# Kernel tuning notes

Hardware: AMD Instinct MI355X
Metric: run time of the kernel (lower is better)

The kernel has to match this reference:

```python
import jax, jax.numpy as jnp
import numpy as np

B, S, D_IN, D_QK, D_V = 4, 4096, 1024, 64, 64

def setup_inputs() -> dict:
    key = jax.random.key(0)
    ks = jax.random.split(key, 8)
    sd = 1.0 / np.sqrt(D_IN)
    return {
        "X": jax.random.normal(ks[0], (B, S, D_IN), dtype=jnp.float32),
        "mask": jnp.ones((B, S, 1), dtype=jnp.float32),
        "Wq": jax.random.uniform(ks[1], (D_IN, D_QK), jnp.float32, -sd, sd),
        "bq": jax.random.uniform(ks[2], (D_QK,), jnp.float32, -sd, sd),
        "Wk": jax.random.uniform(ks[3], (D_IN, D_QK), jnp.float32, -sd, sd),
        "bk": jax.random.uniform(ks[4], (D_QK,), jnp.float32, -sd, sd),
        "Wv": jax.random.uniform(ks[5], (D_IN, D_V), jnp.float32, -sd, sd),
        "bv": jax.random.uniform(ks[6], (D_V,), jnp.float32, -sd, sd),
    }

def reference(X, mask, Wq, bq, Wk, bk, Wv, bv):
    # ReLU-activated projections (no head split, no 1/sqrt(d) scaling)
    q = jax.nn.relu(jnp.einsum('bsd,df->bsf', X, Wq) + bq)   # [B,S,D_QK]
    k = jax.nn.relu(jnp.einsum('bsd,df->bsf', X, Wk) + bk)   # [B,S,D_QK]
    v = jax.nn.relu(jnp.einsum('bsd,df->bsf', X, Wv) + bv)   # [B,S,D_V]
    scores = jax.nn.softmax(jnp.einsum('bqf,bkf->bqk', q, k), axis=-1)  # [B,S,S]
    return jnp.einsum('bqk,bkf->bqf', scores, v) * mask       # mask applied AFTER AV
```

## Files before the change

### kernel.cpp

```cpp
#include <hip/hip_runtime.h>


typedef short s16x8 __attribute__((ext_vector_type(8)));
typedef float fx4   __attribute__((ext_vector_type(4)));
typedef unsigned short u16x4 __attribute__((ext_vector_type(4)));

#define LOG2E 1.4426950408889634f

__device__ __forceinline__ unsigned short f2bf(float x) {
    unsigned int u = __float_as_uint(x);
    u += 0x7FFFu + ((u >> 16) & 1u);
    return (unsigned short)(u >> 16);
}
__device__ __forceinline__ float bf2f(unsigned short b) {
    return __uint_as_float(((unsigned int)b) << 16);
}

__global__ __launch_bounds__(256) void prep_w_kernel(
    const float* __restrict__ Wq, const float* __restrict__ Wk, const float* __restrict__ Wv,
    unsigned short* __restrict__ wt_hi, unsigned short* __restrict__ wt_lo)
{
    __shared__ __align__(16) unsigned short sh[64][72];
    __shared__ __align__(16) unsigned short sl[64][72];

    const int y  = blockIdx.x;
    const int kt = blockIdx.y;
    const float* W = (y == 0) ? Wq : (y == 1) ? Wk : Wv;
    const int t  = threadIdx.x;

    const int kl = t >> 2;
    const int c0 = (t & 3) * 16;
    const float* src = W + (size_t)(kt * 64 + kl) * 64 + c0;
    #pragma unroll
    for (int j = 0; j < 4; j++) {
        fx4 v = *(const fx4*)(src + j * 4);
        #pragma unroll
        for (int i = 0; i < 4; i++) {
            float x = v[i];
            unsigned short h = f2bf(x);
            unsigned short l = f2bf(x - bf2f(h));
            sh[c0 + j * 4 + i][kl] = h;
            sl[c0 + j * 4 + i][kl] = l;
        }
    }
    __syncthreads();

    const int c  = t >> 2;
    const int k0 = (t & 3) * 16;
    size_t o = (size_t)(y * 64 + c) * 1024 + kt * 64 + k0;
    *(s16x8*)(wt_hi + o)     = *(const s16x8*)&sh[c][k0];
    *(s16x8*)(wt_hi + o + 8) = *(const s16x8*)&sh[c][k0 + 8];
    *(s16x8*)(wt_lo + o)     = *(const s16x8*)&sl[c][k0];
    *(s16x8*)(wt_lo + o + 8) = *(const s16x8*)&sl[c][k0 + 8];
}

__global__ __launch_bounds__(512, 4) void proj_kernel(
    const float* __restrict__ X,
    const unsigned short* __restrict__ wt_hi, const unsigned short* __restrict__ wt_lo,
    const float* __restrict__ bq, const float* __restrict__ bk, const float* __restrict__ bv,
    unsigned short* __restrict__ q_hi, unsigned short* __restrict__ q_lo,
    unsigned short* __restrict__ k_bf, unsigned short* __restrict__ vt_g)
{
    __shared__ __align__(16) unsigned short a_buf[2][64][72];
    __shared__ __align__(16) unsigned short b_hi[64][72];
    __shared__ __align__(16) unsigned short b_lo[64][72];

    const int tid  = threadIdx.x;
    const int lane = tid & 63;
    const int w    = tid >> 6;
    const int quad = lane >> 4;
    const int l15  = lane & 15;
    const int rs   = w & 3;
    const int ch   = w >> 2;

    const int f   = blockIdx.x;
    const int xcd = f & 7;
    const int jj  = f >> 3;
    const int y   = jj % 3;
    const int m0  = ((jj / 3) * 8 + xcd) * 64;

    fx4 acc[2];
    acc[0] = (fx4){0.f, 0.f, 0.f, 0.f};
    acc[1] = (fx4){0.f, 0.f, 0.f, 0.f};

    const int xrow = tid >> 4;
    const int xoff = (tid & 15) * 4;
    const int wrow = tid >> 3;
    const int woff = (tid & 7) * 8;

    const float* xb0 = X + (size_t)(m0 + xrow) * 1024 + xoff;
    const float* xb1 = X + (size_t)(m0 + xrow + 32) * 1024 + xoff;
    const size_t wb  = (size_t)(y * 64 + wrow) * 1024 + woff;

    fx4   xr[4][2];
    s16x8 wrh[2], wrl[2];
    #pragma unroll
    for (int d = 0; d < 4; d++) {
        xr[d][0] = *(const fx4*)(xb0 + d * 64);
        xr[d][1] = *(const fx4*)(xb1 + d * 64);
    }
    #pragma unroll
    for (int d = 0; d < 2; d++) {
        wrh[d] = *(const s16x8*)(wt_hi + wb + d * 64);
        wrl[d] = *(const s16x8*)(wt_lo + wb + d * 64);
    }

    #pragma unroll 4
    for (int kc = 0; kc < 16; kc++) {
        if (kc) __syncthreads();
        #pragma unroll
        for (int i = 0; i < 2; i++) {
            fx4 xv = xr[kc & 3][i];
            unsigned short h0 = f2bf(xv.x), h1 = f2bf(xv.y), h2 = f2bf(xv.z), h3 = f2bf(xv.w);
            unsigned short l0 = f2bf(xv.x - bf2f(h0)), l1 = f2bf(xv.y - bf2f(h1));
            unsigned short l2 = f2bf(xv.z - bf2f(h2)), l3 = f2bf(xv.w - bf2f(h3));
            *(u16x4*)&a_buf[0][xrow + i * 32][xoff] = (u16x4){h0, h1, h2, h3};
            *(u16x4*)&a_buf[1][xrow + i * 32][xoff] = (u16x4){l0, l1, l2, l3};
        }
        *(s16x8*)&b_hi[wrow][woff] = wrh[kc & 1];
        *(s16x8*)&b_lo[wrow][woff] = wrl[kc & 1];
        __syncthreads();

        if (kc < 12) {
            xr[kc & 3][0] = *(const fx4*)(xb0 + (kc + 4) * 64);
            xr[kc & 3][1] = *(const fx4*)(xb1 + (kc + 4) * 64);
        }
        if (kc < 14) {
            wrh[kc & 1] = *(const s16x8*)(wt_hi + wb + (kc + 2) * 64);
            wrl[kc & 1] = *(const s16x8*)(wt_lo + wb + (kc + 2) * 64);
        }

        s16x8 ah[2], al[2];
        #pragma unroll
        for (int ks = 0; ks < 2; ks++) {
            int r = rs * 16 + l15;
            ah[ks] = *(const s16x8*)&a_buf[0][r][ks * 32 + quad * 8];
            al[ks] = *(const s16x8*)&a_buf[1][r][ks * 32 + quad * 8];
        }
        #pragma unroll
        for (int nt = 0; nt < 2; nt++) {
            #pragma unroll
            for (int ks = 0; ks < 2; ks++) {
                s16x8 bh = *(const s16x8*)&b_hi[ch * 32 + nt * 16 + l15][ks * 32 + quad * 8];
                s16x8 bl = *(const s16x8*)&b_lo[ch * 32 + nt * 16 + l15][ks * 32 + quad * 8];
                acc[nt] = __builtin_amdgcn_mfma_f32_16x16x32_bf16(ah[ks], bh, acc[nt], 0, 0, 0);
                acc[nt] = __builtin_amdgcn_mfma_f32_16x16x32_bf16(ah[ks], bl, acc[nt], 0, 0, 0);
                acc[nt] = __builtin_amdgcn_mfma_f32_16x16x32_bf16(al[ks], bh, acc[nt], 0, 0, 0);
            }
        }
    }
    __syncthreads();

    const float* bias = (y == 0) ? bq : (y == 1) ? bk : bv;
    const int b   = m0 >> 12;
    const int s0b = m0 & 4095;
    unsigned short* vtr = &a_buf[0][0][0];

    #pragma unroll
    for (int nt = 0; nt < 2; nt++) {
        int col = ch * 32 + nt * 16 + l15;
        float bb = bias[col];
        int rloc = rs * 16 + quad * 4;
        #pragma unroll
        for (int r = 0; r < 4; r++) {
            float v = acc[nt][r] + bb;
            v = fmaxf(v, 0.f);
            size_t grow = (size_t)(m0 + rloc + r);
            if (y == 0) {
                unsigned short h = f2bf(v);
                unsigned short l = f2bf(v - bf2f(h));
                q_hi[grow * 64 + col] = h;
                q_lo[grow * 64 + col] = l;
            } else if (y == 1) {
                k_bf[grow * 64 + col] = f2bf(v);
            } else {
                vtr[col * 72 + rloc + r] = f2bf(v);
            }
        }
    }
    if (y == 2) {
        __syncthreads();
        int row = tid >> 3;
        int off = (tid & 7) * 8;
        s16x8 vv = *(const s16x8*)&vtr[row * 72 + off];
        *(s16x8*)(vt_g + (size_t)(b * 64 + row) * 4096 + s0b + off) = vv;
    }
}

__global__ __launch_bounds__(512, 6) void attn_kernel(
    const unsigned short* __restrict__ q_hi, const unsigned short* __restrict__ q_lo,
    const unsigned short* __restrict__ k_bf, const unsigned short* __restrict__ vt_g,
    unsigned short* __restrict__ pOb, float* __restrict__ pL)
{
    __shared__ __align__(16) unsigned short kt[64][72];
    __shared__ __align__(16) unsigned short vt[64][72];
    __shared__ __align__(16) unsigned short pt[8][16][40];

    const int tid  = threadIdx.x;
    const int lane = tid & 63;
    const int w    = tid >> 6;
    const int quad = lane >> 4;
    const int l15  = lane & 15;
    const int ck   = blockIdx.y;
    const int b    = blockIdx.z;
    const int q0   = blockIdx.x * 128;

    const size_t qoff = ((size_t)b * 4096 + q0 + w * 16 + l15) * 64 + quad * 8;
    s16x8 qh0 = *(const s16x8*)(q_hi + qoff);
    s16x8 qh1 = *(const s16x8*)(q_hi + qoff + 32);
    s16x8 ql0 = *(const s16x8*)(q_lo + qoff);
    s16x8 ql1 = *(const s16x8*)(q_lo + qoff + 32);

    fx4 accO[4];
    #pragma unroll
    for (int nt = 0; nt < 4; nt++) accO[nt] = (fx4){0.f, 0.f, 0.f, 0.f};
    float lsum[4] = {0.f, 0.f, 0.f, 0.f};

    const unsigned short* kgb = k_bf + (size_t)b * 4096 * 64;
    const unsigned short* vgb = vt_g + (size_t)b * 64 * 4096;

    const int srow = tid >> 3;
    const int soff = (tid & 7) * 8;

    const int it0 = ck * 8;
    s16x8 nk = *(const s16x8*)(kgb + (size_t)it0 * 4096 + (size_t)srow * 64 + soff);
    s16x8 nv = *(const s16x8*)(vgb + (size_t)srow * 4096 + it0 * 64 + soff);

    for (int it = it0; it < it0 + 8; it++) {
        *(s16x8*)&kt[srow][soff] = nk;
        *(s16x8*)&vt[srow][soff] = nv;
        __syncthreads();
        if (it + 1 < it0 + 8) {
            nk = *(const s16x8*)(kgb + (size_t)(it + 1) * 4096 + (size_t)srow * 64 + soff);
            nv = *(const s16x8*)(vgb + (size_t)srow * 4096 + (it + 1) * 64 + soff);
        }

        #pragma unroll
        for (int kh = 0; kh < 2; kh++) {
            #pragma unroll
            for (int nt2 = 0; nt2 < 2; nt2++) {
                int key = kh * 32 + nt2 * 16 + l15;
                s16x8 k0 = *(const s16x8*)&kt[key][quad * 8];
                s16x8 k1 = *(const s16x8*)&kt[key][32 + quad * 8];
                fx4 sc = (fx4){0.f, 0.f, 0.f, 0.f};
                __builtin_amdgcn_s_setprio(1);
                sc = __builtin_amdgcn_mfma_f32_16x16x32_bf16(qh0, k0, sc, 0, 0, 0);
                sc = __builtin_amdgcn_mfma_f32_16x16x32_bf16(ql0, k0, sc, 0, 0, 0);
                sc = __builtin_amdgcn_mfma_f32_16x16x32_bf16(qh1, k1, sc, 0, 0, 0);
                sc = __builtin_amdgcn_mfma_f32_16x16x32_bf16(ql1, k1, sc, 0, 0, 0);
                __builtin_amdgcn_s_setprio(0);
                #pragma unroll
                for (int r = 0; r < 4; r++) {
                    float p = __builtin_amdgcn_exp2f(sc[r] * LOG2E);
                    unsigned short pb = f2bf(p);
                    lsum[r] += bf2f(pb);
                    pt[w][quad * 4 + r][nt2 * 16 + l15] = pb;
                }
            }
            s16x8 pa = *(const s16x8*)&pt[w][l15][quad * 8];
            __builtin_amdgcn_s_setprio(1);
            #pragma unroll
            for (int nt = 0; nt < 4; nt++) {
                s16x8 vf = *(const s16x8*)&vt[nt * 16 + l15][kh * 32 + quad * 8];
                accO[nt] = __builtin_amdgcn_mfma_f32_16x16x32_bf16(pa, vf, accO[nt], 0, 0, 0);
            }
            __builtin_amdgcn_s_setprio(0);
        }
        __syncthreads();
    }

    #pragma unroll
    for (int r = 0; r < 4; r++) {
        float v = lsum[r];
        #pragma unroll
        for (int o = 1; o < 16; o <<= 1) v += __shfl_xor(v, o);
        lsum[r] = v;
    }
    #pragma unroll
    for (int r = 0; r < 4; r++) {
        int qrow = q0 + w * 16 + quad * 4 + r;
        size_t grow = (size_t)b * 4096 + qrow;
        #pragma unroll
        for (int nt = 0; nt < 4; nt++)
            pOb[((size_t)ck * 16384 + grow) * 64 + nt * 16 + l15] = f2bf(accO[nt][r]);
        if (l15 == 0)
            pL[(size_t)ck * 16384 + grow] = lsum[r];
    }
}

__global__ __launch_bounds__(256) void combine_kernel(
    const unsigned short* __restrict__ pOb, const float* __restrict__ pL,
    const float* __restrict__ mask, float* __restrict__ out)
{
    int idx = blockIdx.x * 256 + threadIdx.x;
    int q  = idx >> 4;
    int dg = idx & 15;
    fx4 s = (fx4){0.f, 0.f, 0.f, 0.f};
    float l = 0.f;
    #pragma unroll
    for (int c = 0; c < 8; c++) {
        u16x4 h = *(const u16x4*)(pOb + ((size_t)c * 16384 + q) * 64 + dg * 4);
        s.x += bf2f(h.x);
        s.y += bf2f(h.y);
        s.z += bf2f(h.z);
        s.w += bf2f(h.w);
        l += pL[(size_t)c * 16384 + q];
    }
    float scale = mask[q] / l;
    *(fx4*)(out + (size_t)q * 64 + dg * 4) = s * scale;
}

extern "C" void kernel_launch(void* const* d_in, const int* in_sizes, int n_in,
                              void* d_out, int out_size, void* d_ws, size_t ws_size,
                              hipStream_t stream)
{
    const float* X    = (const float*)d_in[0];
    const float* mask = (const float*)d_in[1];
    const float* Wq   = (const float*)d_in[2];
    const float* bq   = (const float*)d_in[3];
    const float* Wk   = (const float*)d_in[4];
    const float* bk   = (const float*)d_in[5];
    const float* Wv   = (const float*)d_in[6];
    const float* bv   = (const float*)d_in[7];
    float* out = (float*)d_out;

    char* ws = (char*)d_ws;
    unsigned short* q_hi  = (unsigned short*)(ws);
    unsigned short* q_lo  = (unsigned short*)(ws + (size_t)(2u << 20));
    unsigned short* k_bf  = (unsigned short*)(ws + (size_t)(4u << 20));
    unsigned short* vt_g  = (unsigned short*)(ws + (size_t)(6u << 20));
    unsigned short* wt_hi = (unsigned short*)(ws + (size_t)(8u << 20));
    unsigned short* wt_lo = (unsigned short*)(ws + (size_t)(8u << 20) + 393216);
    unsigned short* pOb   = (unsigned short*)(ws + (size_t)(9u << 20));
    float*          pL    = (float*)(ws + (size_t)(25u << 20));

    hipLaunchKernelGGL(prep_w_kernel, dim3(3, 16), dim3(256), 0, stream,
                       Wq, Wk, Wv, wt_hi, wt_lo);
    hipLaunchKernelGGL(proj_kernel, dim3(768), dim3(512), 0, stream,
                       X, wt_hi, wt_lo, bq, bk, bv, q_hi, q_lo, k_bf, vt_g);
    hipLaunchKernelGGL(attn_kernel, dim3(32, 8, 4), dim3(512), 0, stream,
                       q_hi, q_lo, k_bf, vt_g, pOb, pL);
    hipLaunchKernelGGL(combine_kernel, dim3(1024), dim3(256), 0, stream,
                       pOb, pL, mask, out);
}
```

Before: 174.1 us.

## Compute Q, K, V projections in one block per row tile to reuse X

Restructures the projection kernel so each 768-thread block computes all three Q/K/V outputs for a 64-row tile, instead of one output per block. X is loaded and split into bf16 hi/lo once rather than three times, and each wave now computes a 32x32 sub-tile. The cost is fewer, larger blocks (256), more shared memory for the full weight slice, and possibly lower occupancy.

New measurement: 166.3 us. 1.05x faster.

```diff
diff --git a/kernel.cpp b/kernel.cpp
--- a/kernel.cpp
+++ b/kernel.cpp
@@ -54,98 +54,115 @@
     *(s16x8*)(wt_lo + o + 8) = *(const s16x8*)&sl[c][k0 + 8];
 }
 
-__global__ __launch_bounds__(512, 4) void proj_kernel(
+__global__ __launch_bounds__(768, 3) void proj_kernel(
     const float* __restrict__ X,
     const unsigned short* __restrict__ wt_hi, const unsigned short* __restrict__ wt_lo,
     const float* __restrict__ bq, const float* __restrict__ bk, const float* __restrict__ bv,
     unsigned short* __restrict__ q_hi, unsigned short* __restrict__ q_lo,
     unsigned short* __restrict__ k_bf, unsigned short* __restrict__ vt_g)
 {
-    __shared__ __align__(16) unsigned short a_buf[2][64][72];
-    __shared__ __align__(16) unsigned short b_hi[64][72];
-    __shared__ __align__(16) unsigned short b_lo[64][72];
+    __shared__ __align__(16) unsigned short a_hi[64][72];
+    __shared__ __align__(16) unsigned short a_lo[64][72];
+    __shared__ __align__(16) unsigned short bsh[192][72];
+    __shared__ __align__(16) unsigned short bsl[192][72];
 
     const int tid  = threadIdx.x;
     const int lane = tid & 63;
     const int w    = tid >> 6;
     const int quad = lane >> 4;
     const int l15  = lane & 15;
-    const int rs   = w & 3;
-    const int ch   = w >> 2;
-
-    const int f   = blockIdx.x;
-    const int xcd = f & 7;
-    const int jj  = f >> 3;
-    const int y   = jj % 3;
-    const int m0  = ((jj / 3) * 8 + xcd) * 64;
-
-    fx4 acc[2];
-    acc[0] = (fx4){0.f, 0.f, 0.f, 0.f};
-    acc[1] = (fx4){0.f, 0.f, 0.f, 0.f};
+    const int rowg = w & 1;
+    const int colg = w >> 1;
+    const int y    = colg >> 1;
+    const int ch   = colg & 1;
+
+    const int m0 = blockIdx.x * 64;
+
+    fx4 acc[2][2];
+    #pragma unroll
+    for (int i = 0; i < 2; i++)
+        #pragma unroll
+        for (int j = 0; j < 2; j++) acc[i][j] = (fx4){0.f, 0.f, 0.f, 0.f};
 
     const int xrow = tid >> 4;
     const int xoff = (tid & 15) * 4;
-    const int wrow = tid >> 3;
-    const int woff = (tid & 7) * 8;
-
     const float* xb0 = X + (size_t)(m0 + xrow) * 1024 + xoff;
     const float* xb1 = X + (size_t)(m0 + xrow + 32) * 1024 + xoff;
-    const size_t wb  = (size_t)(y * 64 + wrow) * 1024 + woff;
+
+    const int wrow = tid >> 2;
+    const int wk   = (tid & 3) * 16;
+    const size_t wb = (size_t)wrow * 1024 + wk;
 
     fx4   xr[4][2];
-    s16x8 wrh[2], wrl[2];
-    #pragma unroll
-    for (int d = 0; d < 4; d++) {
-        xr[d][0] = *(const fx4*)(xb0 + d * 64);
-        xr[d][1] = *(const fx4*)(xb1 + d * 64);
+    s16x8 wrh[2][2], wrl[2][2];
+    if (tid < 512) {
+        #pragma unroll
+        for (int d = 0; d < 4; d++) {
+            xr[d][0] = *(const fx4*)(xb0 + d * 64);
+            xr[d][1] = *(const fx4*)(xb1 + d * 64);
+        }
     }
     #pragma unroll
     for (int d = 0; d < 2; d++) {
-        wrh[d] = *(const s16x8*)(wt_hi + wb + d * 64);
-        wrl[d] = *(const s16x8*)(wt_lo + wb + d * 64);
+        wrh[d][0] = *(const s16x8*)(wt_hi + wb + d * 64);
+        wrh[d][1] = *(const s16x8*)(wt_hi + wb + d * 64 + 8);
+        wrl[d][0] = *(const s16x8*)(wt_lo + wb + d * 64);
+        wrl[d][1] = *(const s16x8*)(wt_lo + wb + d * 64 + 8);
     }
 
     #pragma unroll 4
     for (int kc = 0; kc < 16; kc++) {
         if (kc) __syncthreads();
-        #pragma unroll
-        for (int i = 0; i < 2; i++) {
-            fx4 xv = xr[kc & 3][i];
-            unsigned short h0 = f2bf(xv.x), h1 = f2bf(xv.y), h2 = f2bf(xv.z), h3 = f2bf(xv.w);
-            unsigned short l0 = f2bf(xv.x - bf2f(h0)), l1 = f2bf(xv.y - bf2f(h1));
-            unsigned short l2 = f2bf(xv.z - bf2f(h2)), l3 = f2bf(xv.w - bf2f(h3));
-            *(u16x4*)&a_buf[0][xrow + i * 32][xoff] = (u16x4){h0, h1, h2, h3};
-            *(u16x4*)&a_buf[1][xrow + i * 32][xoff] = (u16x4){l0, l1, l2, l3};
-        }
-        *(s16x8*)&b_hi[wrow][woff] = wrh[kc & 1];
-        *(s16x8*)&b_lo[wrow][woff] = wrl[kc & 1];
+        if (tid < 512) {
+            #pragma unroll
+            for (int i = 0; i < 2; i++) {
+                fx4 xv = xr[kc & 3][i];
+                unsigned short h0 = f2bf(xv.x), h1 = f2bf(xv.y), h2 = f2bf(xv.z), h3 = f2bf(xv.w);
+                unsigned short l0 = f2bf(xv.x - bf2f(h0)), l1 = f2bf(xv.y - bf2f(h1));
+                unsigned short l2 = f2bf(xv.z - bf2f(h2)), l3 = f2bf(xv.w - bf2f(h3));
+                *(u16x4*)&a_hi[xrow + i * 32][xoff] = (u16x4){h0, h1, h2, h3};
+                *(u16x4*)&a_lo[xrow + i * 32][xoff] = (u16x4){l0, l1, l2, l3};
+            }
+        }
+        *(s16x8*)&bsh[wrow][wk]     = wrh[kc & 1][0];
+        *(s16x8*)&bsh[wrow][wk + 8] = wrh[kc & 1][1];
+        *(s16x8*)&bsl[wrow][wk]     = wrl[kc & 1][0];
+        *(s16x8*)&bsl[wrow][wk + 8] = wrl[kc & 1][1];
         __syncthreads();
 
-        if (kc < 12) {
+        if (tid < 512 && kc < 12) {
             xr[kc & 3][0] = *(const fx4*)(xb0 + (kc + 4) * 64);
             xr[kc & 3][1] = *(const fx4*)(xb1 + (kc + 4) * 64);
         }
         if (kc < 14) {
-            wrh[kc & 1] = *(const s16x8*)(wt_hi + wb + (kc + 2) * 64);
-            wrl[kc & 1] = *(const s16x8*)(wt_lo + wb + (kc + 2) * 64);
-        }
-
-        s16x8 ah[2], al[2];
-        #pragma unroll
-        for (int ks = 0; ks < 2; ks++) {
-            int r = rs * 16 + l15;
-            ah[ks] = *(const s16x8*)&a_buf[0][r][ks * 32 + quad * 8];
-            al[ks] = *(const s16x8*)&a_buf[1][r][ks * 32 + quad * 8];
-        }
+            wrh[kc & 1][0] = *(const s16x8*)(wt_hi + wb + (kc + 2) * 64);
+            wrh[kc & 1][1] = *(const s16x8*)(wt_hi + wb + (kc + 2) * 64 + 8);
+            wrl[kc & 1][0] = *(const s16x8*)(wt_lo + wb + (kc + 2) * 64);
+            wrl[kc & 1][1] = *(const s16x8*)(wt_lo + wb + (kc + 2) * 64 + 8);
+        }
+
+        s16x8 ah[2][2], al[2][2];
+        #pragma unroll
+        for (int sub = 0; sub < 2; sub++)
+            #pragma unroll
+            for (int ks = 0; ks < 2; ks++) {
+                const int r = rowg * 32 + sub * 16 + l15;
+                ah[sub][ks] = *(const s16x8*)&a_hi[r][ks * 32 + quad * 8];
+                al[sub][ks] = *(const s16x8*)&a_lo[r][ks * 32 + quad * 8];
+            }
         #pragma unroll
         for (int nt = 0; nt < 2; nt++) {
+            const int br = colg * 32 + nt * 16 + l15;
             #pragma unroll
             for (int ks = 0; ks < 2; ks++) {
-                s16x8 bh = *(const s16x8*)&b_hi[ch * 32 + nt * 16 + l15][ks * 32 + quad * 8];
-                s16x8 bl = *(const s16x8*)&b_lo[ch * 32 + nt * 16 + l15][ks * 32 + quad * 8];
-                acc[nt] = __builtin_amdgcn_mfma_f32_16x16x32_bf16(ah[ks], bh, acc[nt], 0, 0, 0);
-                acc[nt] = __builtin_amdgcn_mfma_f32_16x16x32_bf16(ah[ks], bl, acc[nt], 0, 0, 0);
-                acc[nt] = __builtin_amdgcn_mfma_f32_16x16x32_bf16(al[ks], bh, acc[nt], 0, 0, 0);
+                s16x8 bh = *(const s16x8*)&bsh[br][ks * 32 + quad * 8];
+                s16x8 bl = *(const s16x8*)&bsl[br][ks * 32 + quad * 8];
+                #pragma unroll
+                for (int sub = 0; sub < 2; sub++) {
+                    acc[sub][nt] = __builtin_amdgcn_mfma_f32_16x16x32_bf16(ah[sub][ks], bh, acc[sub][nt], 0, 0, 0);
+                    acc[sub][nt] = __builtin_amdgcn_mfma_f32_16x16x32_bf16(ah[sub][ks], bl, acc[sub][nt], 0, 0, 0);
+                    acc[sub][nt] = __builtin_amdgcn_mfma_f32_16x16x32_bf16(al[sub][ks], bh, acc[sub][nt], 0, 0, 0);
+                }
             }
         }
     }
@@ -154,32 +171,33 @@
     const float* bias = (y == 0) ? bq : (y == 1) ? bk : bv;
     const int b   = m0 >> 12;
     const int s0b = m0 & 4095;
-    unsigned short* vtr = &a_buf[0][0][0];
-
-    #pragma unroll
-    for (int nt = 0; nt < 2; nt++) {
-        int col = ch * 32 + nt * 16 + l15;
-        float bb = bias[col];
-        int rloc = rs * 16 + quad * 4;
-        #pragma unroll
-        for (int r = 0; r < 4; r++) {
-            float v = acc[nt][r] + bb;
-            v = fmaxf(v, 0.f);
-            size_t grow = (size_t)(m0 + rloc + r);
-            if (y == 0) {
-                unsigned short h = f2bf(v);
-                unsigned short l = f2bf(v - bf2f(h));
-                q_hi[grow * 64 + col] = h;
-                q_lo[grow * 64 + col] = l;
-            } else if (y == 1) {
-                k_bf[grow * 64 + col] = f2bf(v);
-            } else {
-                vtr[col * 72 + rloc + r] = f2bf(v);
-            }
-        }
-    }
-    if (y == 2) {
-        __syncthreads();
+    unsigned short* vtr = &a_hi[0][0];
+
+    #pragma unroll
+    for (int sub = 0; sub < 2; sub++)
+        #pragma unroll
+        for (int nt = 0; nt < 2; nt++) {
+            const int col = ch * 32 + nt * 16 + l15;
+            const float bb = bias[col];
+            const int rloc = rowg * 32 + sub * 16 + quad * 4;
+            #pragma unroll
+            for (int r = 0; r < 4; r++) {
+                float v = fmaxf(acc[sub][nt][r] + bb, 0.f);
+                size_t grow = (size_t)(m0 + rloc + r);
+                if (y == 0) {
+                    unsigned short h = f2bf(v);
+                    unsigned short l = f2bf(v - bf2f(h));
+                    q_hi[grow * 64 + col] = h;
+                    q_lo[grow * 64 + col] = l;
+                } else if (y == 1) {
+                    k_bf[grow * 64 + col] = f2bf(v);
+                } else {
+                    vtr[col * 72 + rloc + r] = f2bf(v);
+                }
+            }
+        }
+    __syncthreads();
+    if (tid < 512) {
         int row = tid >> 3;
         int off = (tid & 7) * 8;
         s16x8 vv = *(const s16x8*)&vtr[row * 72 + off];
@@ -336,7 +354,7 @@
 
     hipLaunchKernelGGL(prep_w_kernel, dim3(3, 16), dim3(256), 0, stream,
                        Wq, Wk, Wv, wt_hi, wt_lo);
-    hipLaunchKernelGGL(proj_kernel, dim3(768), dim3(512), 0, stream,
+    hipLaunchKernelGGL(proj_kernel, dim3(256), dim3(768), 0, stream,
                        X, wt_hi, wt_lo, bq, bk, bv, q_hi, q_lo, k_bf, vt_g);
     hipLaunchKernelGGL(attn_kernel, dim3(32, 8, 4), dim3(512), 0, stream,
                        q_hi, q_lo, k_bf, vt_g, pOb, pL);
```
